# Kernel tuning notes

Hardware: AMD Instinct MI355X
Metric: run time of the kernel (lower is better)

Reference implementation:

```python
import jax, jax.numpy as jnp
import numpy as np

C = 256
CQK = C // 8  # query/key projection dim (in_dim // 8)
B, H, W = 4, 64, 64


def setup_inputs() -> dict:
    key = jax.random.key(0)
    ks = jax.random.split(key, 7)
    scale = 0.05
    x = jax.random.normal(ks[0], (B, C, H, W), dtype=jnp.float32)
    Wq = jax.random.normal(ks[1], (CQK, C), dtype=jnp.float32) * scale
    bq = jax.random.normal(ks[2], (CQK,), dtype=jnp.float32) * scale
    Wk = jax.random.normal(ks[3], (CQK, C), dtype=jnp.float32) * scale
    bk = jax.random.normal(ks[4], (CQK,), dtype=jnp.float32) * scale
    Wv = jax.random.normal(ks[5], (C, C), dtype=jnp.float32) * scale
    bv = jax.random.normal(ks[6], (C,), dtype=jnp.float32) * scale
    return {"x": x, "Wq": Wq, "bq": bq, "Wk": Wk, "bk": bk, "Wv": Wv, "bv": bv}


def reference(x, Wq, bq, Wk, bk, Wv, bv):
    b, c, h, w = x.shape
    n = h * w
    xf = x.reshape(b, c, n)  # [B, C, N]
    # 1x1 convs == per-pixel linear maps over channels
    q = jnp.einsum('dc,bcn->bnd', Wq, xf) + bq[None, None, :]   # [B, N, C/8]
    k = jnp.einsum('dc,bcn->bdn', Wk, xf) + bk[None, :, None]   # [B, C/8, N]
    v = jnp.einsum('dc,bcn->bdn', Wv, xf) + bv[None, :, None]   # [B, C, N]
    energy = jnp.einsum('bnd,bdm->bnm', q, k)                    # [B, N, N]
    attention = jax.nn.softmax(energy, axis=-1)                  # softmax over keys
    # out = V @ attention^T  (torch: bmm(proj_value, attention.permute(0,2,1)))
    out = jnp.einsum('bdm,bnm->bdn', v, attention)               # [B, C, N]
    return out.reshape(b, c, h, w) + x
```

## Files before the change

kernel.cpp:

```cpp
#include <hip/hip_runtime.h>
#include <math.h>

#define BATCH 4
#define CH    256
#define NPIX  4096
#define DQK   32

typedef short          s16;
typedef unsigned int   uint_t;
typedef __attribute__((ext_vector_type(8)))  short short8;
typedef __attribute__((ext_vector_type(4)))  float floatx4;
typedef __attribute__((ext_vector_type(16))) float floatx16;

__device__ __forceinline__ s16 f2bf(float f) {
  union { float f; uint_t u; } v; v.f = f;
  return (s16)((v.u + 0x8000u) >> 16);
}
__device__ __forceinline__ float bf2f(s16 u) {
  union { uint_t u; float f; } v; v.u = ((uint_t)(unsigned short)u) << 16; return v.f;
}
__device__ __forceinline__ uint_t pk2(float a, float b) {
  union { float f; uint_t u; } x, y; x.f = a; y.f = b;
  return (((y.u + 0x8000u) >> 16) << 16) | ((x.u + 0x8000u) >> 16);
}

__global__ __launch_bounds__(256) void prepack(
    const float* __restrict__ Wq, const float* __restrict__ bq,
    const float* __restrict__ Wk, const float* __restrict__ bk,
    const float* __restrict__ Wv, const float* __restrict__ bv,
    s16* __restrict__ Wbf, float* __restrict__ Bsw)
{
  const int gid = blockIdx.x * 256 + threadIdx.x;
  const int e0  = gid * 4;
  const int row = e0 >> 8, col = e0 & 255;
  const float* src = (row < 32) ? Wq + (size_t)row * 256
                   : (row < 64) ? Wk + (size_t)(row - 32) * 256
                                : Wv + (size_t)(row - 64) * 256;
  float4 f = *(const float4*)(src + col);
  uint2 o; o.x = pk2(f.x, f.y); o.y = pk2(f.z, f.w);
  *(uint2*)(Wbf + e0) = o;
  if (gid < 320)
    Bsw[gid] = (gid < 32) ? bq[gid] : (gid < 64) ? bk[gid - 32] : bv[gid - 64];
}

__global__ __launch_bounds__(256, 2) void proj_mfma(
    const float* __restrict__ x, const s16* __restrict__ Wbf,
    const float* __restrict__ Bsw,
    s16* __restrict__ Qw, s16* __restrict__ Kw, s16* __restrict__ Vw)
{
  const int b  = blockIdx.x >> 7;
  const int n0 = (blockIdx.x & 127) << 5;
  const int t  = threadIdx.x;

  __shared__ s16 Xs[32][264];
  __shared__ s16 Os[256][40];

  const float* xb = x + (size_t)b * CH * NPIX + n0;
  #pragma unroll
  for (int i = 0; i < 2; ++i) {
    int task = i * 256 + t;
    int ncg  = task & 7;
    int kcg  = task >> 3;
    const float* src = xb + (size_t)(kcg * 4) * NPIX + ncg * 4;
    float rows[4][4];
    *(float4*)&rows[0][0] = *(const float4*)(src);
    *(float4*)&rows[1][0] = *(const float4*)(src + NPIX);
    *(float4*)&rows[2][0] = *(const float4*)(src + 2 * NPIX);
    *(float4*)&rows[3][0] = *(const float4*)(src + 3 * NPIX);
    #pragma unroll
    for (int c = 0; c < 4; ++c) {
      uint2 pk;
      pk.x = pk2(rows[0][c], rows[1][c]);
      pk.y = pk2(rows[2][c], rows[3][c]);
      *(uint2*)&Xs[ncg * 4 + c][kcg * 4] = pk;
    }
  }
  __syncthreads();

  const int w    = t >> 6;
  const int l15  = t & 15;
  const int quad = (t & 63) >> 4;

  floatx4 acc[5][2];
  #pragma unroll
  for (int si = 0; si < 5; ++si)
    #pragma unroll
    for (int nt = 0; nt < 2; ++nt) acc[si][nt] = (floatx4){0.f, 0.f, 0.f, 0.f};

  short8 afc[5], afn[5];
  #pragma unroll
  for (int si = 0; si < 5; ++si) {
    const int s = w + si * 4;
    afc[si] = *(const short8*)(Wbf + (size_t)(s * 16 + l15) * 256 + quad * 8);
  }
  for (int kc = 0; kc < 8; ++kc) {
    const int k0  = kc * 32;
    const int kn0 = (kc < 7) ? k0 + 32 : 0;
    #pragma unroll
    for (int si = 0; si < 5; ++si) {
      const int s = w + si * 4;
      afn[si] = *(const short8*)(Wbf + (size_t)(s * 16 + l15) * 256 + kn0 + quad * 8);
    }
    short8 bf[2];
    #pragma unroll
    for (int nt = 0; nt < 2; ++nt)
      bf[nt] = *(const short8*)&Xs[l15 + 16 * nt][k0 + quad * 8];
    #pragma unroll
    for (int si = 0; si < 5; ++si)
      #pragma unroll
      for (int nt = 0; nt < 2; ++nt)
        acc[si][nt] = __builtin_amdgcn_mfma_f32_16x16x32_bf16(afc[si], bf[nt], acc[si][nt], 0, 0, 0);
    #pragma unroll
    for (int si = 0; si < 5; ++si) afc[si] = afn[si];
  }

  #pragma unroll
  for (int si = 0; si < 5; ++si) {
    const int s = w + si * 4;
    float4 bb = *(const float4*)(Bsw + 16 * s + quad * 4);
    #pragma unroll
    for (int nt = 0; nt < 2; ++nt) {
      const int px  = 16 * nt + l15;
      float v0 = acc[si][nt][0] + bb.x;
      float v1 = acc[si][nt][1] + bb.y;
      float v2 = acc[si][nt][2] + bb.z;
      float v3 = acc[si][nt][3] + bb.w;
      if (s < 4) {
        s16* dst = (s < 2) ? Qw : Kw;
        int d0 = (s & 1) * 16 + quad * 4;
        uint2 pq; pq.x = pk2(v0, v1); pq.y = pk2(v2, v3);
        *(uint2*)(dst + ((size_t)b * NPIX + n0 + px) * DQK + d0) = pq;
      } else {
        const int c0 = (s - 4) * 16 + quad * 4;
        Os[c0 + 0][px] = f2bf(v0);
        Os[c0 + 1][px] = f2bf(v1);
        Os[c0 + 2][px] = f2bf(v2);
        Os[c0 + 3][px] = f2bf(v3);
      }
    }
  }
  __syncthreads();
  #pragma unroll
  for (int rep = 0; rep < 4; ++rep) {
    const int task = rep * 256 + t;
    const int ch   = task >> 2;
    const int seg  = task & 3;
    *(uint4*)(Vw + ((size_t)b * CH + ch) * NPIX + n0 + seg * 8) =
        *(const uint4*)&Os[ch][seg * 8];
  }
}

__global__ __launch_bounds__(512, 4) void attn_mfma(
    const s16* __restrict__ Qw, const s16* __restrict__ Kw,
    const s16* __restrict__ Vw, s16* __restrict__ Op, float* __restrict__ Lp)
{
  const int bi = blockIdx.x;
  const int b  = (bi & 7) >> 1;
  const int ks = (bi >> 3) & 1;
  const int qt = ((bi >> 4) << 1) | (bi & 1);
  const int n0 = qt * 64;
  const int km0 = ks * 2048;
  const int t  = threadIdx.x;
  const int w    = t >> 6;
  const int l15  = t & 15;
  const int quad = (t & 63) >> 4;
  const int l31  = t & 31;
  const int half = (t & 63) >> 5;

  __shared__ s16  Pt[2][64][136];
  __shared__ float Lsum[64][8];

  const s16* qbase = Qw + ((size_t)b * NPIX + n0) * DQK;
  short8 qb[4];
  #pragma unroll
  for (int tq = 0; tq < 4; ++tq)
    qb[tq] = *(const short8*)(qbase + (size_t)(16 * tq + l15) * DQK + quad * 8);

  floatx16 o0, o1;
  #pragma unroll
  for (int i = 0; i < 16; ++i) { o0[i] = 0.f; o1[i] = 0.f; }
  float l_part[4] = {0.f, 0.f, 0.f, 0.f};

  const s16* kbase = Kw + ((size_t)b * NPIX + km0) * DQK;
  const s16* vrow  = Vw + ((size_t)b * CH + 32 * w + l31) * NPIX + km0;

  short8 ka_c = *(const short8*)(kbase + (size_t)(16 * w + l15) * DQK + quad * 8);
  short8 va[8];
  #pragma unroll
  for (int s = 0; s < 8; ++s)
    va[s] = *(const short8*)(vrow + s * 16 + half * 8);

  int buf = 0;
  for (int kt = 0; kt < 16; ++kt) {
    const int m0  = kt * 128;
    const int mn0 = (kt < 15) ? m0 + 128 : 0;

    floatx4 sacc[4];
    #pragma unroll
    for (int tq = 0; tq < 4; ++tq)
      sacc[tq] = __builtin_amdgcn_mfma_f32_16x16x32_bf16(
                   ka_c, qb[tq], (floatx4){0.f, 0.f, 0.f, 0.f}, 0, 0, 0);

    short8 ka_n = *(const short8*)(kbase + (size_t)(mn0 + 16 * w + l15) * DQK + quad * 8);

    #pragma unroll
    for (int tq = 0; tq < 4; ++tq) {
      float p0 = __expf(sacc[tq][0]);
      float p1 = __expf(sacc[tq][1]);
      float p2 = __expf(sacc[tq][2]);
      float p3 = __expf(sacc[tq][3]);
      float ts = (p0 + p1) + (p2 + p3);
      uint2 pk; pk.x = pk2(p0, p1); pk.y = pk2(p2, p3);
      *(uint2*)&Pt[buf][16 * tq + l15][16 * w + quad * 4] = pk;
      ts += __shfl_xor(ts, 16);
      ts += __shfl_xor(ts, 32);
      l_part[tq] += ts;
    }
    __syncthreads();

    #pragma unroll
    for (int s = 0; s < 8; ++s) {
      short8 pb0 = *(const short8*)&Pt[buf][l31][16 * s + half * 8];
      short8 pb1 = *(const short8*)&Pt[buf][32 + l31][16 * s + half * 8];
      o0 = __builtin_amdgcn_mfma_f32_32x32x16_bf16(va[s], pb0, o0, 0, 0, 0);
      o1 = __builtin_amdgcn_mfma_f32_32x32x16_bf16(va[s], pb1, o1, 0, 0, 0);
      va[s] = *(const short8*)(vrow + mn0 + 16 * s + half * 8);
    }
    ka_c = ka_n;
    buf ^= 1;
  }

  if (quad == 0) {
    #pragma unroll
    for (int tq = 0; tq < 4; ++tq) Lsum[16 * tq + l15][w] = l_part[tq];
  }
  __syncthreads();
  if (t < 64) {
    float4 s0 = *(const float4*)&Lsum[t][0];
    float4 s1 = *(const float4*)&Lsum[t][4];
    Lp[(((size_t)b * 2 + ks) * 64 + qt) * 64 + t] =
        ((s0.x + s0.y) + (s0.z + s0.w)) + ((s1.x + s1.y) + (s1.z + s1.w));
  }

  s16* ob = Op + (((size_t)b * 2 + ks) * 64 + qt) * (256 * 64);
  #pragma unroll
  for (int reg = 0; reg < 16; ++reg) {
    const int ch = 32 * w + (reg & 3) + 8 * (reg >> 2) + 4 * half;
    ob[ch * 64 + l31]      = f2bf(o0[reg]);
    ob[ch * 64 + 32 + l31] = f2bf(o1[reg]);
  }
}

__global__ __launch_bounds__(256) void reduce_merge(
    const s16* __restrict__ Op, const float* __restrict__ Lp,
    const float* __restrict__ x, float* __restrict__ out)
{
  const size_t e0 = ((size_t)blockIdx.x * 256 + threadIdx.x) * 8;
  const int n  = (int)(e0 & 4095);
  const int ch = (int)((e0 >> 12) & 255);
  const int b  = (int)(e0 >> 20);
  const int qt = n >> 6, q = n & 63;

  const size_t p0 = (((size_t)b * 2 + 0) * 64 + qt) * (256 * 64) + ch * 64 + q;
  const size_t p1 = (((size_t)b * 2 + 1) * 64 + qt) * (256 * 64) + ch * 64 + q;
  union { uint4 v; s16 u[8]; } O0, O1;
  O0.v = *(const uint4*)(Op + p0);
  O1.v = *(const uint4*)(Op + p1);

  const float* l0p = Lp + (((size_t)b * 2 + 0) * 64 + qt) * 64 + q;
  const float* l1p = Lp + (((size_t)b * 2 + 1) * 64 + qt) * 64 + q;
  float4 l0a = *(const float4*)l0p, l0b = *(const float4*)(l0p + 4);
  float4 l1a = *(const float4*)l1p, l1b = *(const float4*)(l1p + 4);
  float linv[8] = {
    1.f / (l0a.x + l1a.x), 1.f / (l0a.y + l1a.y),
    1.f / (l0a.z + l1a.z), 1.f / (l0a.w + l1a.w),
    1.f / (l0b.x + l1b.x), 1.f / (l0b.y + l1b.y),
    1.f / (l0b.z + l1b.z), 1.f / (l0b.w + l1b.w) };

  float4 xa = *(const float4*)(x + e0), xb = *(const float4*)(x + e0 + 4);
  float r[8] = { xa.x, xa.y, xa.z, xa.w, xb.x, xb.y, xb.z, xb.w };
  #pragma unroll
  for (int j = 0; j < 8; ++j)
    r[j] = fmaf(bf2f(O0.u[j]) + bf2f(O1.u[j]), linv[j], r[j]);
  *(float4*)(out + e0)     = make_float4(r[0], r[1], r[2], r[3]);
  *(float4*)(out + e0 + 4) = make_float4(r[4], r[5], r[6], r[7]);
}

extern "C" void kernel_launch(void* const* d_in, const int* in_sizes, int n_in,
                              void* d_out, int out_size, void* d_ws, size_t ws_size,
                              hipStream_t stream) {
  (void)in_sizes; (void)n_in; (void)out_size; (void)ws_size;
  const float* x  = (const float*)d_in[0];
  const float* Wq = (const float*)d_in[1];
  const float* bq = (const float*)d_in[2];
  const float* Wk = (const float*)d_in[3];
  const float* bk = (const float*)d_in[4];
  const float* Wv = (const float*)d_in[5];
  const float* bv = (const float*)d_in[6];
  float* out = (float*)d_out;

  unsigned char* ws = (unsigned char*)d_ws;
  s16*   Qw  = (s16*)ws;
  s16*   Kw  = (s16*)(ws + (size_t)1 * 1024 * 1024);
  s16*   Vw  = (s16*)(ws + (size_t)2 * 1024 * 1024);
  s16*   Wbf = (s16*)(ws + (size_t)10 * 1024 * 1024);
  float* Bsw = (float*)(ws + (size_t)10 * 1024 * 1024 + 256 * 1024);
  float* Lp  = (float*)(ws + (size_t)10 * 1024 * 1024 + 512 * 1024);
  s16*   Op  = (s16*)(ws + (size_t)11 * 1024 * 1024);

  hipLaunchKernelGGL(prepack, dim3(80), dim3(256), 0, stream,
                     Wq, bq, Wk, bk, Wv, bv, Wbf, Bsw);
  hipLaunchKernelGGL(proj_mfma, dim3(512), dim3(256), 0, stream,
                     x, Wbf, Bsw, Qw, Kw, Vw);
  hipLaunchKernelGGL(attn_mfma, dim3(512), dim3(512), 0, stream,
                     Qw, Kw, Vw, Op, Lp);
  hipLaunchKernelGGL(reduce_merge, dim3(2048), dim3(256), 0, stream,
                     Op, Lp, x, out);
}
```

Baseline: 165.1 us.

## Split projection into transpose-to-bf16 pass and LDS-free MFMA projection kernel

The fused projection kernel, which staged x through LDS, is replaced by two kernels. A separate xtrans kernel transposes x into a pixel-major bf16 buffer. A new proj2 kernel then reads MFMA operands directly from global memory, using weights prepacked in a k-chunked transposed layout, with more blocks (1024) and higher occupancy. The aim is to remove LDS staging and the strided fp32 loads from the projection GEMM. In exchange it adds an extra kernel launch and a round trip of the bf16 copy of x through memory. The Q/K outputs are now written as scalar 2-byte stores, and Xt aliases the Op workspace region, which is only safe because the two are used in different kernels.

```diff
diff --git a/kernel.cpp b/kernel.cpp
--- a/kernel.cpp
+++ b/kernel.cpp
@@ -24,129 +24,126 @@
   return (((y.u + 0x8000u) >> 16) << 16) | ((x.u + 0x8000u) >> 16);
 }
 
-__global__ __launch_bounds__(256) void prepack(
+__global__ __launch_bounds__(256) void prepack2(
     const float* __restrict__ Wq, const float* __restrict__ bq,
     const float* __restrict__ Wk, const float* __restrict__ bk,
     const float* __restrict__ Wv, const float* __restrict__ bv,
-    s16* __restrict__ Wbf, float* __restrict__ Bsw)
+    s16* __restrict__ Wt, float* __restrict__ Bsw)
 {
   const int gid = blockIdx.x * 256 + threadIdx.x;
-  const int e0  = gid * 4;
-  const int row = e0 >> 8, col = e0 & 255;
-  const float* src = (row < 32) ? Wq + (size_t)row * 256
-                   : (row < 64) ? Wk + (size_t)(row - 32) * 256
-                                : Wv + (size_t)(row - 64) * 256;
-  float4 f = *(const float4*)(src + col);
-  uint2 o; o.x = pk2(f.x, f.y); o.y = pk2(f.z, f.w);
-  *(uint2*)(Wbf + e0) = o;
+  const int kc  = gid / 320;
+  const int n   = gid - kc * 320;
+  const float* src = (n < 32) ? Wq + (size_t)n * 256
+                   : (n < 64) ? Wk + (size_t)(n - 32) * 256
+                              : Wv + (size_t)(n - 64) * 256;
+  float4 f0 = *(const float4*)(src + kc * 8);
+  float4 f1 = *(const float4*)(src + kc * 8 + 4);
+  uint4 o;
+  o.x = pk2(f0.x, f0.y); o.y = pk2(f0.z, f0.w);
+  o.z = pk2(f1.x, f1.y); o.w = pk2(f1.z, f1.w);
+  *(uint4*)(Wt + (size_t)gid * 8) = o;
   if (gid < 320)
     Bsw[gid] = (gid < 32) ? bq[gid] : (gid < 64) ? bk[gid - 32] : bv[gid - 64];
 }
 
-__global__ __launch_bounds__(256, 2) void proj_mfma(
-    const float* __restrict__ x, const s16* __restrict__ Wbf,
+__global__ __launch_bounds__(256) void xtrans(
+    const float* __restrict__ x, s16* __restrict__ Xt)
+{
+  const int bi = blockIdx.x;
+  const int b  = bi >> 8;
+  const int c0 = ((bi >> 6) & 3) * 64;
+  const int n0 = (bi & 63) * 64;
+  const int t  = threadIdx.x;
+
+  __shared__ float Ls[64][65];
+
+  const float* xb = x + ((size_t)b * CH + c0) * NPIX + n0;
+  #pragma unroll
+  for (int rep = 0; rep < 4; ++rep) {
+    const int task = rep * 256 + t;
+    const int pg = task & 15, c = task >> 4;
+    float4 f = *(const float4*)(xb + (size_t)c * NPIX + pg * 4);
+    Ls[c][pg * 4 + 0] = f.x; Ls[c][pg * 4 + 1] = f.y;
+    Ls[c][pg * 4 + 2] = f.z; Ls[c][pg * 4 + 3] = f.w;
+  }
+  __syncthreads();
+
+  s16* xo = Xt + ((size_t)b * NPIX + n0) * CH + c0;
+  #pragma unroll
+  for (int rep = 0; rep < 2; ++rep) {
+    const int cg = t & 7;
+    const int n  = (t >> 3) + rep * 32;
+    float f[8];
+    #pragma unroll
+    for (int j = 0; j < 8; ++j) f[j] = Ls[cg * 8 + j][n];
+    uint4 o;
+    o.x = pk2(f[0], f[1]); o.y = pk2(f[2], f[3]);
+    o.z = pk2(f[4], f[5]); o.w = pk2(f[6], f[7]);
+    *(uint4*)(xo + (size_t)n * CH + cg * 8) = o;
+  }
+}
+
+__global__ __launch_bounds__(256, 4) void proj2(
+    const s16* __restrict__ Xt, const s16* __restrict__ Wt,
     const float* __restrict__ Bsw,
     s16* __restrict__ Qw, s16* __restrict__ Kw, s16* __restrict__ Vw)
 {
-  const int b  = blockIdx.x >> 7;
-  const int n0 = (blockIdx.x & 127) << 5;
+  const int bi = blockIdx.x;
+  const int b    = bi & 3;
+  const int tile = (bi >> 2) & 63;
+  const int os   = bi >> 8;
   const int t  = threadIdx.x;
-
-  __shared__ s16 Xs[32][264];
-  __shared__ s16 Os[256][40];
-
-  const float* xb = x + (size_t)b * CH * NPIX + n0;
-  #pragma unroll
-  for (int i = 0; i < 2; ++i) {
-    int task = i * 256 + t;
-    int ncg  = task & 7;
-    int kcg  = task >> 3;
-    const float* src = xb + (size_t)(kcg * 4) * NPIX + ncg * 4;
-    float rows[4][4];
-    *(float4*)&rows[0][0] = *(const float4*)(src);
-    *(float4*)&rows[1][0] = *(const float4*)(src + NPIX);
-    *(float4*)&rows[2][0] = *(const float4*)(src + 2 * NPIX);
-    *(float4*)&rows[3][0] = *(const float4*)(src + 3 * NPIX);
-    #pragma unroll
-    for (int c = 0; c < 4; ++c) {
-      uint2 pk;
-      pk.x = pk2(rows[0][c], rows[1][c]);
-      pk.y = pk2(rows[2][c], rows[3][c]);
-      *(uint2*)&Xs[ncg * 4 + c][kcg * 4] = pk;
-    }
-  }
-  __syncthreads();
-
   const int w    = t >> 6;
   const int l15  = t & 15;
   const int quad = (t & 63) >> 4;
 
-  floatx4 acc[5][2];
-  #pragma unroll
-  for (int si = 0; si < 5; ++si)
-    #pragma unroll
-    for (int nt = 0; nt < 2; ++nt) acc[si][nt] = (floatx4){0.f, 0.f, 0.f, 0.f};
-
-  short8 afc[5], afn[5];
-  #pragma unroll
-  for (int si = 0; si < 5; ++si) {
-    const int s = w + si * 4;
-    afc[si] = *(const short8*)(Wbf + (size_t)(s * 16 + l15) * 256 + quad * 8);
-  }
+  const int pxw = tile * 64 + 16 * w;
+  const int ro0 = os * 80;
+
+  const s16* abase = Xt + ((size_t)b * NPIX + pxw + l15) * CH + quad * 8;
+  const s16* bbase = Wt + ((size_t)quad * 320 + ro0 + l15) * 8;
+
+  floatx4 acc[5];
+  #pragma unroll
+  for (int st = 0; st < 5; ++st) acc[st] = (floatx4){0.f, 0.f, 0.f, 0.f};
+
+  short8 Ac, An, Bc[5], Bn[5];
+  Ac = *(const short8*)(abase);
+  #pragma unroll
+  for (int st = 0; st < 5; ++st)
+    Bc[st] = *(const short8*)(bbase + (size_t)st * 128);
+
   for (int kc = 0; kc < 8; ++kc) {
-    const int k0  = kc * 32;
-    const int kn0 = (kc < 7) ? k0 + 32 : 0;
-    #pragma unroll
-    for (int si = 0; si < 5; ++si) {
-      const int s = w + si * 4;
-      afn[si] = *(const short8*)(Wbf + (size_t)(s * 16 + l15) * 256 + kn0 + quad * 8);
+    const int kn = (kc < 7) ? kc + 1 : 7;
+    An = *(const short8*)(abase + kn * 32);
+    #pragma unroll
+    for (int st = 0; st < 5; ++st)
+      Bn[st] = *(const short8*)(bbase + (size_t)kn * 10240 + (size_t)st * 128);
+    #pragma unroll
+    for (int st = 0; st < 5; ++st)
+      acc[st] = __builtin_amdgcn_mfma_f32_16x16x32_bf16(Ac, Bc[st], acc[st], 0, 0, 0);
+    Ac = An;
+    #pragma unroll
+    for (int st = 0; st < 5; ++st) Bc[st] = Bn[st];
+  }
+
+  #pragma unroll
+  for (int st = 0; st < 5; ++st) {
+    const int orow = ro0 + 16 * st + l15;
+    const float bias = Bsw[orow];
+    float v0 = acc[st][0] + bias, v1 = acc[st][1] + bias;
+    float v2 = acc[st][2] + bias, v3 = acc[st][3] + bias;
+    const int px = pxw + quad * 4;
+    if (orow < 64) {
+      s16* dst = (orow < 32) ? Qw : Kw;
+      const int d = orow & 31;
+      s16* p = dst + ((size_t)b * NPIX + px) * DQK + d;
+      p[0] = f2bf(v0); p[DQK] = f2bf(v1); p[2 * DQK] = f2bf(v2); p[3 * DQK] = f2bf(v3);
+    } else {
+      const int ch = orow - 64;
+      uint2 o; o.x = pk2(v0, v1); o.y = pk2(v2, v3);
+      *(uint2*)(Vw + ((size_t)b * CH + ch) * NPIX + px) = o;
     }
-    short8 bf[2];
-    #pragma unroll
-    for (int nt = 0; nt < 2; ++nt)
-      bf[nt] = *(const short8*)&Xs[l15 + 16 * nt][k0 + quad * 8];
-    #pragma unroll
-    for (int si = 0; si < 5; ++si)
-      #pragma unroll
-      for (int nt = 0; nt < 2; ++nt)
-        acc[si][nt] = __builtin_amdgcn_mfma_f32_16x16x32_bf16(afc[si], bf[nt], acc[si][nt], 0, 0, 0);
-    #pragma unroll
-    for (int si = 0; si < 5; ++si) afc[si] = afn[si];
-  }
-
-  #pragma unroll
-  for (int si = 0; si < 5; ++si) {
-    const int s = w + si * 4;
-    float4 bb = *(const float4*)(Bsw + 16 * s + quad * 4);
-    #pragma unroll
-    for (int nt = 0; nt < 2; ++nt) {
-      const int px  = 16 * nt + l15;
-      float v0 = acc[si][nt][0] + bb.x;
-      float v1 = acc[si][nt][1] + bb.y;
-      float v2 = acc[si][nt][2] + bb.z;
-      float v3 = acc[si][nt][3] + bb.w;
-      if (s < 4) {
-        s16* dst = (s < 2) ? Qw : Kw;
-        int d0 = (s & 1) * 16 + quad * 4;
-        uint2 pq; pq.x = pk2(v0, v1); pq.y = pk2(v2, v3);
-        *(uint2*)(dst + ((size_t)b * NPIX + n0 + px) * DQK + d0) = pq;
-      } else {
-        const int c0 = (s - 4) * 16 + quad * 4;
-        Os[c0 + 0][px] = f2bf(v0);
-        Os[c0 + 1][px] = f2bf(v1);
-        Os[c0 + 2][px] = f2bf(v2);
-        Os[c0 + 3][px] = f2bf(v3);
-      }
-    }
-  }
-  __syncthreads();
-  #pragma unroll
-  for (int rep = 0; rep < 4; ++rep) {
-    const int task = rep * 256 + t;
-    const int ch   = task >> 2;
-    const int seg  = task & 3;
-    *(uint4*)(Vw + ((size_t)b * CH + ch) * NPIX + n0 + seg * 8) =
-        *(const uint4*)&Os[ch][seg * 8];
   }
 }
 
@@ -303,15 +300,17 @@
   s16*   Qw  = (s16*)ws;
   s16*   Kw  = (s16*)(ws + (size_t)1 * 1024 * 1024);
   s16*   Vw  = (s16*)(ws + (size_t)2 * 1024 * 1024);
-  s16*   Wbf = (s16*)(ws + (size_t)10 * 1024 * 1024);
+  s16*   Wt  = (s16*)(ws + (size_t)10 * 1024 * 1024);
   float* Bsw = (float*)(ws + (size_t)10 * 1024 * 1024 + 256 * 1024);
   float* Lp  = (float*)(ws + (size_t)10 * 1024 * 1024 + 512 * 1024);
+  s16*   Xt  = (s16*)(ws + (size_t)11 * 1024 * 1024);
   s16*   Op  = (s16*)(ws + (size_t)11 * 1024 * 1024);
 
-  hipLaunchKernelGGL(prepack, dim3(80), dim3(256), 0, stream,
-                     Wq, bq, Wk, bk, Wv, bv, Wbf, Bsw);
-  hipLaunchKernelGGL(proj_mfma, dim3(512), dim3(256), 0, stream,
-                     x, Wbf, Bsw, Qw, Kw, Vw);
+  hipLaunchKernelGGL(prepack2, dim3(40), dim3(256), 0, stream,
+                     Wq, bq, Wk, bk, Wv, bv, Wt, Bsw);
+  hipLaunchKernelGGL(xtrans, dim3(1024), dim3(256), 0, stream, x, Xt);
+  hipLaunchKernelGGL(proj2, dim3(1024), dim3(256), 0, stream,
+                     Xt, Wt, Bsw, Qw, Kw, Vw);
   hipLaunchKernelGGL(attn_mfma, dim3(512), dim3(512), 0, stream,
                      Qw, Kw, Vw, Op, Lp);
   hipLaunchKernelGGL(reduce_merge, dim3(2048), dim3(256), 0, stream,
```

Measured after the change: 167.7 us. Within noise of the previous version (+1.6%).
